# Kernel tuning notes

Measured on AMD Instinct MI355X. Metric: run time of the kernel, lower is better.

Reference implementation:

```python
import jax, jax.numpy as jnp
import numpy as np

N_NODES = 50000
N_EDGES = 800000
IN_DIM = 128
OUT_DIM = 64


def setup_inputs() -> dict:
    key = jax.random.key(0)
    k1, k2, k3, k4, k5 = jax.random.split(key, 5)
    h = jax.random.normal(k1, (N_NODES, IN_DIM), dtype=jnp.float32)
    # Xavier-normal-ish scale for weights
    W_w = jax.random.normal(k2, (IN_DIM, OUT_DIM), dtype=jnp.float32) * (2.0 / (IN_DIM + OUT_DIM)) ** 0.5
    W_b = jnp.zeros((OUT_DIM,), dtype=jnp.float32)
    A_w = jax.random.normal(k3, (2 * OUT_DIM, 1), dtype=jnp.float32) * (2.0 / (2 * OUT_DIM + 1)) ** 0.5
    A_b = jnp.zeros((1,), dtype=jnp.float32)
    src = jax.random.randint(k4, (N_EDGES,), 0, N_NODES, dtype=jnp.int32)
    dst = jax.random.randint(k5, (N_EDGES,), 0, N_NODES, dtype=jnp.int32)
    return {"h": h, "W_w": W_w, "W_b": W_b, "A_w": A_w, "A_b": A_b, "src": src, "dst": dst}


def reference(h, W_w, W_b, A_w, A_b, src, dst):
    n = h.shape[0]
    # Node projection: Wh = W(h)
    Wh = h @ W_w + W_b  # [N, D]
    # Attention logit e_ij = LeakyReLU(A([Wh_i; Wh_j])), computed as node-level
    # partial scores gathered per edge (same math as concat-linear, far less traffic).
    a_dst = (Wh @ A_w[:OUT_DIM, 0])  # [N] -> contribution of Wh_i (dst)
    a_src = (Wh @ A_w[OUT_DIM:, 0])  # [N] -> contribution of Wh_j (src)
    e = jax.nn.leaky_relu(a_dst[dst] + a_src[src] + A_b[0], negative_slope=0.2)  # [E]
    # Segment softmax over incoming edges of each destination node (stable).
    m = jax.ops.segment_max(e, dst, num_segments=n)  # [N], -inf for isolated nodes
    m = jnp.where(jnp.isfinite(m), m, 0.0)
    ex = jnp.exp(e - m[dst])  # [E]
    den = jax.ops.segment_sum(ex, dst, num_segments=n)  # [N]
    alpha = ex / den[dst]  # [E]
    # Weighted scatter-sum aggregate: h_i = sum_j alpha_ij * Wh_j
    out = jax.ops.segment_sum(alpha[:, None] * Wh[src], dst, num_segments=n)  # [N, D]
    # Dropout (p=0.6) is identity in eval mode; omitted for determinism.
    return out
```

## Files before the change

### kernel.cpp

```cpp
#include <hip/hip_runtime.h>
#include <hip/hip_fp16.h>

#define IN_DIM 128
#define OUT_DIM 64
#define MAXDEG 64

typedef __attribute__((ext_vector_type(8))) short short8v;
typedef __attribute__((ext_vector_type(4))) float float4v;
typedef unsigned short ushort_t;
typedef unsigned int uint_t;

__device__ inline ushort_t f_to_bf16(float f) {
    uint_t x = __float_as_uint(f);
    uint_t r = (x + 0x7fffu + ((x >> 16) & 1u)) >> 16;
    return (ushort_t)r;
}

__global__ __launch_bounds__(256) void k_fused(
    const float* __restrict__ h, const float* __restrict__ W,
    const float* __restrict__ Wb, const float* __restrict__ Aw,
    ushort_t* __restrict__ Whb, float* __restrict__ a_dst_arr,
    float* __restrict__ a_src_arr, int N,
    const int* __restrict__ src, const int* __restrict__ dst,
    int* __restrict__ cnt, ushort_t* __restrict__ csr2, int E, int SB)
{
    __shared__ ushort_t Wl[16 * 64 * 8];
    const int t = threadIdx.x;

    if ((int)blockIdx.x < SB) {
        int base = ((int)blockIdx.x * 256 + t) * 4;
        if (base + 4 <= E) {
            int4 s4 = *(const int4*)&src[base];
            int4 d4 = *(const int4*)&dst[base];
            int p0 = atomicAdd(&cnt[d4.x], 1);
            int p1 = atomicAdd(&cnt[d4.y], 1);
            int p2 = atomicAdd(&cnt[d4.z], 1);
            int p3 = atomicAdd(&cnt[d4.w], 1);
            csr2[d4.x * MAXDEG + p0] = (ushort_t)s4.x;
            csr2[d4.y * MAXDEG + p1] = (ushort_t)s4.y;
            csr2[d4.z * MAXDEG + p2] = (ushort_t)s4.z;
            csr2[d4.w * MAXDEG + p3] = (ushort_t)s4.w;
        } else {
            for (int e = base; e < E; e++) {
                int p = atomicAdd(&cnt[dst[e]], 1);
                csr2[dst[e] * MAXDEG + p] = (ushort_t)src[e];
            }
        }
        return;
    }

    stage_w: ;
    {
        int f = t * 32;
        #pragma unroll
        for (int i = 0; i < 32; i++, f++) {
            int frag = f >> 9;
            int ln   = (f >> 3) & 63;
            int j    = f & 7;
            int k    = (frag >> 2) * 32 + (ln >> 4) * 8 + j;
            int d    = (frag & 3) * 16 + (ln & 15);
            Wl[f] = f_to_bf16(W[k * OUT_DIM + d]);
        }
    }
    __syncthreads();

    const int lane = t & 63;
    const int quad = lane >> 4;
    const int col  = lane & 15;
    const int pb   = (int)blockIdx.x - SB;
    const int node0 = (pb * 4 + (t >> 6)) * 16;
    if (node0 >= N) return;

    const int rowc = min(node0 + col, N - 1);
    const float* __restrict__ arow = h + (size_t)rowc * IN_DIM;

    float4v acc[4];
    #pragma unroll
    for (int db = 0; db < 4; db++) acc[db] = (float4v){0.f, 0.f, 0.f, 0.f};

    #pragma unroll
    for (int kb = 0; kb < 4; kb++) {
        const float* ap = arow + kb * 32 + quad * 8;
        float4 a0 = *(const float4*)ap;
        float4 a1 = *(const float4*)(ap + 4);
        union { short8v v; ushort_t u[8]; } af;
        af.u[0] = f_to_bf16(a0.x); af.u[1] = f_to_bf16(a0.y);
        af.u[2] = f_to_bf16(a0.z); af.u[3] = f_to_bf16(a0.w);
        af.u[4] = f_to_bf16(a1.x); af.u[5] = f_to_bf16(a1.y);
        af.u[6] = f_to_bf16(a1.z); af.u[7] = f_to_bf16(a1.w);
        #pragma unroll
        for (int db = 0; db < 4; db++) {
            short8v bf = *(const short8v*)&Wl[(((kb << 2) | db) * 64 + lane) * 8];
            acc[db] = __builtin_amdgcn_mfma_f32_16x16x32_bf16(af.v, bf, acc[db], 0, 0, 0);
        }
    }

    float pd[4] = {0.f, 0.f, 0.f, 0.f};
    float ps[4] = {0.f, 0.f, 0.f, 0.f};
    #pragma unroll
    for (int db = 0; db < 4; db++) {
        float wbv = Wb[db * 16 + col];
        float awd = Aw[db * 16 + col];
        float aws = Aw[OUT_DIM + db * 16 + col];
        #pragma unroll
        for (int r = 0; r < 4; r++) {
            float v = acc[db][r] + wbv;
            int node = node0 + quad * 4 + r;
            if (node < N)
                Whb[(size_t)node * OUT_DIM + db * 16 + col] = f_to_bf16(v);
            pd[r] = fmaf(v, awd, pd[r]);
            ps[r] = fmaf(v, aws, ps[r]);
        }
    }
    #pragma unroll
    for (int r = 0; r < 4; r++) {
        float d_ = pd[r], s_ = ps[r];
        #pragma unroll
        for (int off = 1; off < 16; off <<= 1) {
            d_ += __shfl_xor(d_, off);
            s_ += __shfl_xor(s_, off);
        }
        int node = node0 + quad * 4 + r;
        if (col == 0 && node < N) {
            a_dst_arr[node] = d_;
            a_src_arr[node] = s_;
        }
    }
}

__global__ __launch_bounds__(256) void k_agg(
    const int* __restrict__ cnt, const ushort_t* __restrict__ csr2,
    const uint_t* __restrict__ Whb2,
    const float* __restrict__ a_dst_arr, const float* __restrict__ a_src_arr,
    const float* __restrict__ Ab, float* __restrict__ out, int N)
{
    int node = (int)((blockIdx.x * blockDim.x + threadIdx.x) >> 6);
    int lane = threadIdx.x & 63;
    if (node >= N) return;
    int u = __builtin_amdgcn_readfirstlane(node);
    int deg = cnt[u];
    const ushort_t* __restrict__ seg = csr2 + (size_t)u * MAXDEG;
    const float au = a_dst_arr[u] + Ab[0];

    const int el = lane >> 5;
    const int dl = lane & 31;

    float accx = 0.f, accy = 0.f, wsum = 0.f;
    int j = 0;
    for (; j + 8 <= deg; j += 8) {
        ushort4 r4 = *(const ushort4*)&seg[j + el * 4];
        ushort_t rr[4] = {r4.x, r4.y, r4.z, r4.w};
        #pragma unroll
        for (int b = 0; b < 4; b++) {
            int s = (int)rr[b];
            float v = au + a_src_arr[s];
            v = (v > 0.0f) ? v : 0.2f * v;
            float w = __expf(v);
            uint_t p = Whb2[(size_t)s * 32 + dl];
            float fx = __uint_as_float(p << 16);
            float fy = __uint_as_float(p & 0xffff0000u);
            accx = fmaf(w, fx, accx);
            accy = fmaf(w, fy, accy);
            wsum += w;
        }
    }
    for (; j < deg; j += 2) {
        int e = j + el;
        if (e < deg) {
            int s = (int)seg[e];
            float v = au + a_src_arr[s];
            v = (v > 0.0f) ? v : 0.2f * v;
            float w = __expf(v);
            uint_t p = Whb2[(size_t)s * 32 + dl];
            float fx = __uint_as_float(p << 16);
            float fy = __uint_as_float(p & 0xffff0000u);
            accx = fmaf(w, fx, accx);
            accy = fmaf(w, fy, accy);
            wsum += w;
        }
    }

    accx += __shfl_xor(accx, 32);
    accy += __shfl_xor(accy, 32);
    wsum += __shfl_xor(wsum, 32);

    float inv = (deg > 0) ? 1.0f / wsum : 0.0f;
    if (lane < 32) {
        float2 o = make_float2(accx * inv, accy * inv);
        *(float2*)&out[(size_t)u * OUT_DIM + dl * 2] = o;
    }
}


extern "C" void kernel_launch(void* const* d_in, const int* in_sizes, int n_in,
                              void* d_out, int out_size, void* d_ws, size_t ws_size,
                              hipStream_t stream)
{
    const float* h   = (const float*)d_in[0];
    const float* W_w = (const float*)d_in[1];
    const float* W_b = (const float*)d_in[2];
    const float* A_w = (const float*)d_in[3];
    const float* A_b = (const float*)d_in[4];
    const int*   src = (const int*)d_in[5];
    const int*   dst = (const int*)d_in[6];
    float* out = (float*)d_out;

    int N = in_sizes[0] / IN_DIM;
    int E = in_sizes[5];

    ushort_t* Whb   = (ushort_t*)d_ws;
    float* a_dst_a  = (float*)(Whb + (size_t)N * OUT_DIM);
    float* a_src_a  = a_dst_a + N;
    int*   cnt      = (int*)(a_src_a + N);
    ushort_t* csr2  = (ushort_t*)(cnt + N);

    (void)hipMemsetAsync(cnt, 0, (size_t)N * sizeof(int), stream);

    {
        int SB = (E + 1023) / 1024;
        int ntiles = (N + 15) / 16;
        int PB = (ntiles + 3) / 4;
        k_fused<<<SB + PB, 256, 0, stream>>>(h, W_w, W_b, A_w, Whb,
                                             a_dst_a, a_src_a, N,
                                             src, dst, cnt, csr2, E, SB);
    }
    {
        int grid = (N + 3) / 4;
        k_agg<<<grid, 256, 0, stream>>>(cnt, csr2, (const uint_t*)Whb,
                                        a_dst_a, a_src_a, A_b, out, N);
    }
}
```

Before: 177.7 us.

## Split CSR build into rank-counting and separate nontemporal scatter kernel with persistent grid

The fused kernel no longer writes csr2 inside the atomic pass. It now records per-edge ranks from the atomicAdd on dst counts into a rank array, and a new k_scatter kernel later writes source ids into csr2 with nontemporal stores. k_fused becomes a fixed 1024-block grid-stride kernel: each block first does atomics over strided edge quads, then handles projection tiles in a loop. The aim is to decouple the scattered writes from the atomic latency chain and to balance the atomic and GEMM work across all blocks. In exchange it adds a kernel launch plus a read and write of a 4-byte rank per edge.

```diff
diff --git a/kernel.cpp b/kernel.cpp
--- a/kernel.cpp
+++ b/kernel.cpp
@@ -21,35 +21,14 @@
     const float* __restrict__ Wb, const float* __restrict__ Aw,
     ushort_t* __restrict__ Whb, float* __restrict__ a_dst_arr,
     float* __restrict__ a_src_arr, int N,
-    const int* __restrict__ src, const int* __restrict__ dst,
-    int* __restrict__ cnt, ushort_t* __restrict__ csr2, int E, int SB)
+    const int* __restrict__ dst, int* __restrict__ cnt,
+    int* __restrict__ rank, int E)
 {
     __shared__ ushort_t Wl[16 * 64 * 8];
-    const int t = threadIdx.x;
-
-    if ((int)blockIdx.x < SB) {
-        int base = ((int)blockIdx.x * 256 + t) * 4;
-        if (base + 4 <= E) {
-            int4 s4 = *(const int4*)&src[base];
-            int4 d4 = *(const int4*)&dst[base];
-            int p0 = atomicAdd(&cnt[d4.x], 1);
-            int p1 = atomicAdd(&cnt[d4.y], 1);
-            int p2 = atomicAdd(&cnt[d4.z], 1);
-            int p3 = atomicAdd(&cnt[d4.w], 1);
-            csr2[d4.x * MAXDEG + p0] = (ushort_t)s4.x;
-            csr2[d4.y * MAXDEG + p1] = (ushort_t)s4.y;
-            csr2[d4.z * MAXDEG + p2] = (ushort_t)s4.z;
-            csr2[d4.w * MAXDEG + p3] = (ushort_t)s4.w;
-        } else {
-            for (int e = base; e < E; e++) {
-                int p = atomicAdd(&cnt[dst[e]], 1);
-                csr2[dst[e] * MAXDEG + p] = (ushort_t)src[e];
-            }
-        }
-        return;
-    }
-
-    stage_w: ;
+    const int t   = threadIdx.x;
+    const int bid = (int)blockIdx.x;
+    const int nbk = (int)gridDim.x;
+
     {
         int f = t * 32;
         #pragma unroll
@@ -64,67 +43,105 @@
     }
     __syncthreads();
 
-    const int lane = t & 63;
-    const int quad = lane >> 4;
-    const int col  = lane & 15;
-    const int pb   = (int)blockIdx.x - SB;
-    const int node0 = (pb * 4 + (t >> 6)) * 16;
-    if (node0 >= N) return;
-
-    const int rowc = min(node0 + col, N - 1);
-    const float* __restrict__ arow = h + (size_t)rowc * IN_DIM;
-
-    float4v acc[4];
-    #pragma unroll
-    for (int db = 0; db < 4; db++) acc[db] = (float4v){0.f, 0.f, 0.f, 0.f};
-
-    #pragma unroll
-    for (int kb = 0; kb < 4; kb++) {
-        const float* ap = arow + kb * 32 + quad * 8;
-        float4 a0 = *(const float4*)ap;
-        float4 a1 = *(const float4*)(ap + 4);
-        union { short8v v; ushort_t u[8]; } af;
-        af.u[0] = f_to_bf16(a0.x); af.u[1] = f_to_bf16(a0.y);
-        af.u[2] = f_to_bf16(a0.z); af.u[3] = f_to_bf16(a0.w);
-        af.u[4] = f_to_bf16(a1.x); af.u[5] = f_to_bf16(a1.y);
-        af.u[6] = f_to_bf16(a1.z); af.u[7] = f_to_bf16(a1.w);
-        #pragma unroll
-        for (int db = 0; db < 4; db++) {
-            short8v bf = *(const short8v*)&Wl[(((kb << 2) | db) * 64 + lane) * 8];
-            acc[db] = __builtin_amdgcn_mfma_f32_16x16x32_bf16(af.v, bf, acc[db], 0, 0, 0);
-        }
-    }
-
-    float pd[4] = {0.f, 0.f, 0.f, 0.f};
-    float ps[4] = {0.f, 0.f, 0.f, 0.f};
-    #pragma unroll
-    for (int db = 0; db < 4; db++) {
-        float wbv = Wb[db * 16 + col];
-        float awd = Aw[db * 16 + col];
-        float aws = Aw[OUT_DIM + db * 16 + col];
-        #pragma unroll
-        for (int r = 0; r < 4; r++) {
-            float v = acc[db][r] + wbv;
-            int node = node0 + quad * 4 + r;
-            if (node < N)
-                Whb[(size_t)node * OUT_DIM + db * 16 + col] = f_to_bf16(v);
-            pd[r] = fmaf(v, awd, pd[r]);
-            ps[r] = fmaf(v, aws, ps[r]);
-        }
-    }
-    #pragma unroll
-    for (int r = 0; r < 4; r++) {
-        float d_ = pd[r], s_ = ps[r];
-        #pragma unroll
-        for (int off = 1; off < 16; off <<= 1) {
-            d_ += __shfl_xor(d_, off);
-            s_ += __shfl_xor(s_, off);
-        }
-        int node = node0 + quad * 4 + r;
-        if (col == 0 && node < N) {
-            a_dst_arr[node] = d_;
-            a_src_arr[node] = s_;
-        }
+    {
+        const int gtid = bid * 256 + t;
+        const int nth  = nbk * 256;
+        const int nq   = E >> 2;
+        for (int q = gtid; q < nq; q += nth) {
+            int base = q << 2;
+            int4 d4 = *(const int4*)&dst[base];
+            int r0 = atomicAdd(&cnt[d4.x], 1);
+            int r1 = atomicAdd(&cnt[d4.y], 1);
+            int r2 = atomicAdd(&cnt[d4.z], 1);
+            int r3 = atomicAdd(&cnt[d4.w], 1);
+            *(int4*)&rank[base] = make_int4(r0, r1, r2, r3);
+        }
+        int rem = E & 3, tb = nq << 2;
+        if (gtid < rem) rank[tb + gtid] = atomicAdd(&cnt[dst[tb + gtid]], 1);
+    }
+
+    {
+        const int lane = t & 63;
+        const int quad = lane >> 4;
+        const int col  = lane & 15;
+        const int ntiles = (N + 15) >> 4;
+        for (int tile = bid * 4 + (t >> 6); tile < ntiles; tile += nbk * 4) {
+            const int node0 = tile * 16;
+            const int rowc = min(node0 + col, N - 1);
+            const float* __restrict__ arow = h + (size_t)rowc * IN_DIM;
+
+            float4v acc[4];
+            #pragma unroll
+            for (int db = 0; db < 4; db++) acc[db] = (float4v){0.f, 0.f, 0.f, 0.f};
+
+            #pragma unroll
+            for (int kb = 0; kb < 4; kb++) {
+                const float* ap = arow + kb * 32 + quad * 8;
+                float4 a0 = *(const float4*)ap;
+                float4 a1 = *(const float4*)(ap + 4);
+                union { short8v v; ushort_t u[8]; } af;
+                af.u[0] = f_to_bf16(a0.x); af.u[1] = f_to_bf16(a0.y);
+                af.u[2] = f_to_bf16(a0.z); af.u[3] = f_to_bf16(a0.w);
+                af.u[4] = f_to_bf16(a1.x); af.u[5] = f_to_bf16(a1.y);
+                af.u[6] = f_to_bf16(a1.z); af.u[7] = f_to_bf16(a1.w);
+                #pragma unroll
+                for (int db = 0; db < 4; db++) {
+                    short8v bf = *(const short8v*)&Wl[(((kb << 2) | db) * 64 + lane) * 8];
+                    acc[db] = __builtin_amdgcn_mfma_f32_16x16x32_bf16(af.v, bf, acc[db], 0, 0, 0);
+                }
+            }
+
+            float pd[4] = {0.f, 0.f, 0.f, 0.f};
+            float ps[4] = {0.f, 0.f, 0.f, 0.f};
+            #pragma unroll
+            for (int db = 0; db < 4; db++) {
+                float wbv = Wb[db * 16 + col];
+                float awd = Aw[db * 16 + col];
+                float aws = Aw[OUT_DIM + db * 16 + col];
+                #pragma unroll
+                for (int r = 0; r < 4; r++) {
+                    float v = acc[db][r] + wbv;
+                    int node = node0 + quad * 4 + r;
+                    if (node < N)
+                        Whb[(size_t)node * OUT_DIM + db * 16 + col] = f_to_bf16(v);
+                    pd[r] = fmaf(v, awd, pd[r]);
+                    ps[r] = fmaf(v, aws, ps[r]);
+                }
+            }
+            #pragma unroll
+            for (int r = 0; r < 4; r++) {
+                float d_ = pd[r], s_ = ps[r];
+                #pragma unroll
+                for (int off = 1; off < 16; off <<= 1) {
+                    d_ += __shfl_xor(d_, off);
+                    s_ += __shfl_xor(s_, off);
+                }
+                int node = node0 + quad * 4 + r;
+                if (col == 0 && node < N) {
+                    a_dst_arr[node] = d_;
+                    a_src_arr[node] = s_;
+                }
+            }
+        }
+    }
+}
+
+__global__ __launch_bounds__(256) void k_scatter(
+    const int* __restrict__ src, const int* __restrict__ dst,
+    const int* __restrict__ rank, ushort_t* __restrict__ csr2, int E)
+{
+    int base = (int)(blockIdx.x * blockDim.x + threadIdx.x) * 4;
+    if (base + 4 <= E) {
+        int4 s4 = *(const int4*)&src[base];
+        int4 t4 = *(const int4*)&dst[base];
+        int4 k4 = *(const int4*)&rank[base];
+        __builtin_nontemporal_store((ushort_t)s4.x, &csr2[t4.x * MAXDEG + k4.x]);
+        __builtin_nontemporal_store((ushort_t)s4.y, &csr2[t4.y * MAXDEG + k4.y]);
+        __builtin_nontemporal_store((ushort_t)s4.z, &csr2[t4.z * MAXDEG + k4.z]);
+        __builtin_nontemporal_store((ushort_t)s4.w, &csr2[t4.w * MAXDEG + k4.w]);
+    } else {
+        for (int e = base; e < E; e++)
+            __builtin_nontemporal_store((ushort_t)src[e], &csr2[dst[e] * MAXDEG + rank[e]]);
     }
 }
 
@@ -212,17 +229,19 @@
     float* a_dst_a  = (float*)(Whb + (size_t)N * OUT_DIM);
     float* a_src_a  = a_dst_a + N;
     int*   cnt      = (int*)(a_src_a + N);
-    ushort_t* csr2  = (ushort_t*)(cnt + N);
+    int*   rank     = cnt + N;
+    ushort_t* csr2  = (ushort_t*)(rank + E);
 
     (void)hipMemsetAsync(cnt, 0, (size_t)N * sizeof(int), stream);
 
     {
-        int SB = (E + 1023) / 1024;
-        int ntiles = (N + 15) / 16;
-        int PB = (ntiles + 3) / 4;
-        k_fused<<<SB + PB, 256, 0, stream>>>(h, W_w, W_b, A_w, Whb,
-                                             a_dst_a, a_src_a, N,
-                                             src, dst, cnt, csr2, E, SB);
+        k_fused<<<1024, 256, 0, stream>>>(h, W_w, W_b, A_w, Whb,
+                                          a_dst_a, a_src_a, N,
+                                          dst, cnt, rank, E);
+    }
+    {
+        int grid = (E / 4 + 255) / 256;
+        k_scatter<<<grid, 256, 0, stream>>>(src, dst, rank, csr2, E);
     }
     {
         int grid = (N + 3) / 4;
```

Result: no change. 177.7 us (+0.0%).
